# Optimization experiments

Measured on AMD Instinct MI355X. Metric: run time of the kernel, lower is better.

## Reference

```python
import jax, jax.numpy as jnp
import numpy as np

# ---- config (JambaConfig defaults) ----
D_MODEL = 2048
D_STATE = 128
D_CONV = 4
EXPAND = 2
HEADDIM = 64
D_INNER = EXPAND * D_MODEL           # 4096
NHEADS = D_INNER // HEADDIM          # 64
CONV_DIM = D_INNER + 2 * D_STATE     # 4352
IN_PROJ = 2 * D_INNER + 2 * D_STATE + NHEADS  # 8512
INTER = 5632                         # ((2048*8/3)+255)//256*256
EPS = 1e-6
CHUNK = 128                          # SSD chunk length


def rmsnorm(x, w, eps=EPS):
    var = jnp.mean(jnp.square(x), axis=-1, keepdims=True)
    return x * jax.lax.rsqrt(var + eps) * w


def dw_causal_conv(x, w, b):
    # x: [B,L,C], w: [C,K] depthwise, b: [C]; causal (left pad K-1)
    xt = jnp.transpose(x, (0, 2, 1))                       # [B,C,L]
    xt = jnp.pad(xt, ((0, 0), (0, 0), (D_CONV - 1, 0)))
    y = jax.lax.conv_general_dilated(
        xt, w[:, None, :], window_strides=(1,), padding='VALID',
        feature_group_count=w.shape[0], dimension_numbers=('NCH', 'OIH', 'NCH'))
    y = y + b[None, :, None]
    return jnp.transpose(y, (0, 2, 1))                     # [B,L,C]


def segsum(x):
    # x: [..., T] -> [..., T, T] with out[l,s] = sum_{s<i<=l} x[i], -inf above diag
    T = x.shape[-1]
    xx = jnp.broadcast_to(x[..., None], (*x.shape, T))     # xx[...,i,j] = x[...,i]
    xx = jnp.where(jnp.tril(jnp.ones((T, T), bool), -1), xx, 0.0)
    s = jnp.cumsum(xx, axis=-2)
    return jnp.where(jnp.tril(jnp.ones((T, T), bool), 0), s, -jnp.inf)


def ssd(x, dt, A, Bm, Cm):
    # Mamba2 SSD (chunked selective scan). x:[b,l,h,p] dt:[b,l,h] A:[h] Bm/Cm:[b,l,n]
    b, l, h, p = x.shape
    n = Bm.shape[-1]
    c = l // CHUNK
    xr = x.reshape(b, c, CHUNK, h, p)
    dtr = dt.reshape(b, c, CHUNK, h)
    Br = Bm.reshape(b, c, CHUNK, n)
    Cr = Cm.reshape(b, c, CHUNK, n)
    dA = jnp.transpose(dtr * A, (0, 3, 1, 2))              # [b,h,c,q], all <= 0
    A_cum = jnp.cumsum(dA, axis=-1)                        # [b,h,c,q]
    L = jnp.exp(segsum(dA))                                # [b,h,c,q,q] lower-tri decays
    xdt = xr * dtr[..., None]                              # [b,c,q,h,p]
    # intra-chunk (diagonal blocks)
    Y_diag = jnp.einsum('bcln,bcsn,bhcls,bcshp->bclhp', Cr, Br, L, xdt)
    # chunk-final states
    decay_states = jnp.exp(A_cum[..., -1:] - A_cum)        # [b,h,c,q]
    states = jnp.einsum('bcln,bhcl,bclhp->bchpn', Br, decay_states, xdt)
    # inter-chunk recurrence (parallel via decay matrix over chunks)
    A_last = A_cum[..., -1]                                # [b,h,c]
    decay_chunk = jnp.exp(segsum(jnp.pad(A_last, ((0, 0), (0, 0), (1, 0)))))  # [b,h,c+1,c+1]
    states_cat = jnp.concatenate([jnp.zeros_like(states[:, :1]), states], axis=1)  # [b,c+1,h,p,n]
    new_states = jnp.einsum('bhzc,bchpn->bzhpn', decay_chunk, states_cat)
    prev = new_states[:, :-1]                              # state entering each chunk
    state_decay = jnp.exp(A_cum)                           # [b,h,c,q]
    Y_off = jnp.einsum('bcln,bchpn,bhcl->bclhp', Cr, prev, state_decay)
    return (Y_diag + Y_off).reshape(b, l, h, p)


def setup_inputs() -> dict:
    key = jax.random.key(0)
    ks = jax.random.split(key, 10)
    B, L = 2, 2048
    s = 0.02
    return {
        'hidden_states': jax.random.normal(ks[0], (B, L, D_MODEL), jnp.float32),
        'norm1_w': jnp.ones((D_MODEL,), jnp.float32),
        'in_proj_w': jax.random.normal(ks[1], (D_MODEL, IN_PROJ), jnp.float32) * s,
        'conv_w': jax.random.normal(ks[2], (CONV_DIM, D_CONV), jnp.float32) * 0.1,
        'conv_b': jnp.zeros((CONV_DIM,), jnp.float32),
        'dt_bias': jax.random.uniform(ks[3], (NHEADS,), jnp.float32, -4.0, -1.0),
        'A_log': jnp.log(jnp.arange(1, NHEADS + 1, dtype=jnp.float32)),
        'D_param': jnp.ones((NHEADS,), jnp.float32),
        'mixer_norm_w': jnp.ones((D_INNER,), jnp.float32),
        'out_proj_w': jax.random.normal(ks[4], (D_INNER, D_MODEL), jnp.float32) * s,
        'norm2_w': jnp.ones((D_MODEL,), jnp.float32),
        'gate_w': jax.random.normal(ks[5], (D_MODEL, INTER), jnp.float32) * s,
        'up_w': jax.random.normal(ks[6], (D_MODEL, INTER), jnp.float32) * s,
        'down_w': jax.random.normal(ks[7], (INTER, D_MODEL), jnp.float32) * s,
    }


def reference(hidden_states, norm1_w, in_proj_w, conv_w, conv_b, dt_bias, A_log,
              D_param, mixer_norm_w, out_proj_w, norm2_w, gate_w, up_w, down_w):
    B, L, _ = hidden_states.shape
    # --- norm1 + Mamba2 mixer + residual ---
    res = hidden_states
    h = rmsnorm(hidden_states, norm1_w)
    zxbcdt = h @ in_proj_w                                  # [B,L,8512]
    z = zxbcdt[..., :D_INNER]
    xBC = zxbcdt[..., D_INNER:D_INNER + CONV_DIM]
    dt = jax.nn.softplus(zxbcdt[..., -NHEADS:] + dt_bias)   # [B,L,H]
    xBC = jax.nn.silu(dw_causal_conv(xBC, conv_w, conv_b))
    xs = xBC[..., :D_INNER].reshape(B, L, NHEADS, HEADDIM)
    Bm = xBC[..., D_INNER:D_INNER + D_STATE]
    Cm = xBC[..., D_INNER + D_STATE:]
    A = -jnp.exp(A_log)
    y = ssd(xs, dt, A, Bm, Cm)
    y = y + D_param[None, None, :, None] * xs               # skip D term
    y = y.reshape(B, L, D_INNER)
    y = rmsnorm(y * jax.nn.silu(z), mixer_norm_w)           # gated RMSNorm
    h1 = res + y @ out_proj_w
    # --- norm2 + SwiGLU MLP + residual ---
    h2 = rmsnorm(h1, norm2_w)
    mlp = (jax.nn.silu(h2 @ gate_w) * (h2 @ up_w)) @ down_w
    return h1 + mlp
```

## Files before the change

kernel.cpp:

```cpp
#include <hip/hip_runtime.h>

#define LTOT 2048
#define BATCH 2
#define NTOK 4096
#define DMODEL 2048
#define DSTATE 128
#define NH 64
#define HD 64
#define DINNER 4096
#define CONVD 4352
#define XDTC 4416
#define INP 8512
#define INTER_ 5632
#define CHUNK_ 128
#define NCH 16
#define EPSF 1e-6f

typedef __bf16 bf16x8 __attribute__((ext_vector_type(8)));
typedef float f32x4 __attribute__((ext_vector_type(4)));
typedef unsigned short u16x4 __attribute__((ext_vector_type(4)));
typedef unsigned short u16x8 __attribute__((ext_vector_type(8)));

__device__ __forceinline__ unsigned short f2b(float f){
  unsigned int u = __builtin_bit_cast(unsigned int, f);
  u += 0x7fffu + ((u >> 16) & 1u);
  return (unsigned short)(u >> 16);
}
__device__ __forceinline__ float b2f(unsigned short h){
  return __builtin_bit_cast(float, ((unsigned int)h) << 16);
}
__device__ __forceinline__ f32x4 mfma16(bf16x8 a, bf16x8 b, f32x4 c){
  return __builtin_amdgcn_mfma_f32_16x16x32_bf16(a, b, c, 0, 0, 0);
}
typedef const __attribute__((address_space(1))) void* gas_t;
typedef __attribute__((address_space(3))) void* las_t;
__device__ __forceinline__ void gload16(const void* g, void* l){
  __builtin_amdgcn_global_load_lds((gas_t)g, (las_t)l, 16, 0, 0);
}

__global__ __launch_bounds__(256) void wconv_kernel(const float* __restrict__ W,
                                                    unsigned short* __restrict__ WT,
                                                    int K, int N)
{
  __shared__ unsigned short t[64][72];
  int n0 = blockIdx.x * 64, k0 = blockIdx.y * 64;
  int tid = threadIdx.x;
  int kl = tid >> 4, nl4 = (tid & 15) * 4;
  #pragma unroll
  for (int it = 0; it < 4; it++){
    int kk = kl + it * 16;
    float4 v = make_float4(0.f, 0.f, 0.f, 0.f);
    if (n0 < N) v = *(const float4*)&W[(size_t)(k0 + kk) * N + n0 + nl4];
    t[nl4 + 0][kk] = f2b(v.x);
    t[nl4 + 1][kk] = f2b(v.y);
    t[nl4 + 2][kk] = f2b(v.z);
    t[nl4 + 3][kk] = f2b(v.w);
  }
  __syncthreads();
  int nr = tid >> 3, k8 = (tid & 7) * 8;
  #pragma unroll
  for (int it = 0; it < 2; it++){
    int nn = nr + it * 32;
    *(u16x8*)&WT[(size_t)(n0 + nn) * K + k0 + k8] = *(const u16x8*)&t[nn][k8];
  }
}

__global__ __launch_bounds__(256) void rms_kernel(const float* __restrict__ x,
                                                  const float* __restrict__ w,
                                                  unsigned short* __restrict__ out, int width)
{
  int row = blockIdx.x, tid = threadIdx.x;
  const float* xr = x + (size_t)row * width;
  unsigned short* orow = out + (size_t)row * width;
  int nv = width >> 2;
  float ss = 0.f;
  for (int i = tid; i < nv; i += 256){
    float4 v = ((const float4*)xr)[i];
    ss += v.x*v.x + v.y*v.y + v.z*v.z + v.w*v.w;
  }
  #pragma unroll
  for (int off = 32; off > 0; off >>= 1) ss += __shfl_down(ss, off, 64);
  __shared__ float red[4];
  if ((tid & 63) == 0) red[tid >> 6] = ss;
  __syncthreads();
  float tot = red[0] + red[1] + red[2] + red[3];
  float scale = rsqrtf(tot / (float)width + EPSF);
  for (int i = tid; i < nv; i += 256){
    float4 v = ((const float4*)xr)[i];
    float4 wv = ((const float4*)w)[i];
    u16x4 o = { f2b(v.x * scale * wv.x), f2b(v.y * scale * wv.y),
                f2b(v.z * scale * wv.z), f2b(v.w * scale * wv.w) };
    ((u16x4*)orow)[i] = o;
  }
}

__global__ __launch_bounds__(256) void rms_gated_kernel(const float* __restrict__ y,
                                                        const unsigned short* __restrict__ z,
                                                        const float* __restrict__ w,
                                                        unsigned short* __restrict__ out)
{
  int row = blockIdx.x, tid = threadIdx.x;
  const float* yr = y + (size_t)row * DINNER;
  const unsigned short* zr = z + (size_t)row * DINNER;
  unsigned short* orow = out + (size_t)row * DINNER;
  float g[16];
  float ss = 0.f;
  #pragma unroll
  for (int ii = 0; ii < 4; ii++){
    int i = tid + ii * 256;
    float4 yv = ((const float4*)yr)[i];
    u16x4 zv = ((const u16x4*)zr)[i];
    #pragma unroll
    for (int e = 0; e < 4; e++){
      float zf = b2f(zv[e]);
      float yf = (&yv.x)[e];
      float gg = yf * (zf / (1.f + expf(-zf)));
      g[ii * 4 + e] = gg;
      ss += gg * gg;
    }
  }
  #pragma unroll
  for (int off = 32; off > 0; off >>= 1) ss += __shfl_down(ss, off, 64);
  __shared__ float red[4];
  if ((tid & 63) == 0) red[tid >> 6] = ss;
  __syncthreads();
  float tot = red[0] + red[1] + red[2] + red[3];
  float scale = rsqrtf(tot / (float)DINNER + EPSF);
  #pragma unroll
  for (int ii = 0; ii < 4; ii++){
    int i = tid + ii * 256;
    float4 wv = ((const float4*)w)[i];
    u16x4 o;
    #pragma unroll
    for (int e = 0; e < 4; e++) o[e] = f2b(g[ii * 4 + e] * scale * (&wv.x)[e]);
    ((u16x4*)orow)[i] = o;
  }
}

__global__ __launch_bounds__(256) void act_kernel(unsigned short* __restrict__ g,
                                                  const unsigned short* __restrict__ u, int n8)
{
  int stride = gridDim.x * 256;
  for (int i = blockIdx.x * 256 + threadIdx.x; i < n8; i += stride){
    u16x8 gv = ((const u16x8*)g)[i];
    u16x8 uv = ((const u16x8*)u)[i];
    u16x8 o;
    #pragma unroll
    for (int e = 0; e < 8; e++){
      float gf = b2f(gv[e]);
      o[e] = f2b(gf / (1.f + expf(-gf)) * b2f(uv[e]));
    }
    ((u16x8*)g)[i] = o;
  }
}

__global__ __launch_bounds__(512, 2) void gemm3_kernel(const unsigned short* __restrict__ A,
                                                       const unsigned short* __restrict__ BT,
                                                       const float* __restrict__ addsrc,
                                                       float* __restrict__ Cf,
                                                       unsigned short* __restrict__ Cb,
                                                       unsigned short* __restrict__ Cb2, int splitN,
                                                       const unsigned short* __restrict__ gate,
                                                       float* __restrict__ dtraw,
                                                       int M, int N, int K)
{
  extern __shared__ unsigned short lds[];
  int tid = threadIdx.x, lane = tid & 63, w = tid >> 6;
  int wm = w >> 2, wn = w & 3;
  int bid = blockIdx.x + blockIdx.y * gridDim.x;
  int nwg = gridDim.x * gridDim.y;
  int q8 = nwg >> 3, r8 = nwg & 7;
  int xcd = bid & 7, boff = bid >> 3;
  int wgid = (xcd < r8 ? xcd * (q8 + 1) : r8 * (q8 + 1) + (xcd - r8) * q8) + boff;
  int bn = (wgid % gridDim.x) * 256;
  int bm = (wgid / gridDim.x) * 128;

  int soct8 = ((lane & 3) ^ ((lane >> 2) & 3)) << 3;
  int prow_l = (lane >> 2);
  int ko = (((lane >> 4) ^ (lane & 3)) << 3);
  int rsel = (lane & 15) * 32 + ko;

  f32x4 acc[4][4] = {};
  int NT = K >> 5;

  #define STAGE(kt, bsel)                                                              \
    {                                                                                  \
      unsigned short* bb_ = &lds[(bsel) * 12288];                                      \
      size_t k0_ = (size_t)(kt) << 5;                                                  \
      gload16(&A [(size_t)(bm +       w * 16 + prow_l) * K + k0_ + soct8], &bb_[w * 512]);            \
      gload16(&BT[(size_t)(bn +       w * 16 + prow_l) * K + k0_ + soct8], &bb_[4096 + w * 512]);     \
      gload16(&BT[(size_t)(bn + 128 + w * 16 + prow_l) * K + k0_ + soct8], &bb_[8192 + w * 512]);     \
    }

  STAGE(0, 0)
  STAGE(1, 1)
  asm volatile("s_waitcnt vmcnt(3)" ::: "memory");
  __builtin_amdgcn_s_barrier();
  asm volatile("" ::: "memory");

  for (int t = 0; t < NT; ++t){
    const unsigned short* bufc = &lds[(t % 3) * 12288];
    bf16x8 afr[4], bfr[4];
    #pragma unroll
    for (int i = 0; i < 4; ++i)
      afr[i] = *(const bf16x8*)&bufc[(wm * 64 + i * 16) * 32 + rsel];
    #pragma unroll
    for (int c = 0; c < 4; ++c)
      bfr[c] = *(const bf16x8*)&bufc[4096 + (wn * 64 + c * 16) * 32 + rsel];
    if (t + 2 < NT) STAGE(t + 2, (t + 2) % 3)
    __builtin_amdgcn_s_setprio(1);
    #pragma unroll
    for (int i = 0; i < 4; ++i)
      #pragma unroll
      for (int c = 0; c < 4; ++c)
        acc[i][c] = mfma16(afr[i], bfr[c], acc[i][c]);
    __builtin_amdgcn_s_setprio(0);
    if (t + 2 < NT)      asm volatile("s_waitcnt vmcnt(3)" ::: "memory");
    else if (t + 1 < NT) asm volatile("s_waitcnt vmcnt(0)" ::: "memory");
    asm volatile("" ::: "memory");
    __builtin_amdgcn_s_barrier();
    asm volatile("" ::: "memory");
  }
  #undef STAGE

  int r0 = bm + wm * 64 + ((lane >> 4) << 2);
  int c0 = bn + wn * 64 + (lane & 15);
  #pragma unroll
  for (int i = 0; i < 4; ++i){
    #pragma unroll
    for (int j = 0; j < 4; ++j){
      int cc = c0 + j * 16;
      if (cc < N){
        #pragma unroll
        for (int e = 0; e < 4; ++e){
          int rr = r0 + i * 16 + e;
          float v = acc[i][j][e];
          if (Cf){
            size_t idx = (size_t)rr * N + cc;
            if (addsrc) v += addsrc[idx];
            Cf[idx] = v;
          } else if (cc < splitN){
            size_t idx = (size_t)rr * splitN + cc;
            float vv = v;
            if (gate){ float gg = b2f(gate[idx]); vv = gg / (1.f + expf(-gg)) * v; }
            Cb[idx] = f2b(vv);
          } else {
            Cb2[(size_t)rr * (N - splitN) + (cc - splitN)] = f2b(v);
            if (dtraw && cc >= N - NH) dtraw[(size_t)rr * NH + (cc - (N - NH))] = v;
          }
        }
      }
    }
  }
}

__global__ __launch_bounds__(256, 3) void gemm4_kernel(const unsigned short* __restrict__ A,
                                                       const unsigned short* __restrict__ BT,
                                                       const float* __restrict__ addsrc,
                                                       float* __restrict__ Cf,
                                                       int M, int N, int K)
{
  extern __shared__ unsigned short lds[];
  int tid = threadIdx.x, lane = tid & 63, w = tid >> 6;
  int wm = w >> 1, wn = w & 1;
  int bid = blockIdx.x + blockIdx.y * gridDim.x;
  int nwg = gridDim.x * gridDim.y;
  int q8 = nwg >> 3, r8 = nwg & 7;
  int xcd = bid & 7, boff = bid >> 3;
  int wgid = (xcd < r8 ? xcd * (q8 + 1) : r8 * (q8 + 1) + (xcd - r8) * q8) + boff;
  int bn = (wgid % gridDim.x) * 128;
  int bm = (wgid / gridDim.x) * 128;

  int soct8 = ((lane & 3) ^ ((lane >> 2) & 3)) << 3;
  int prow_l = (lane >> 2);
  int ko = (((lane >> 4) ^ (lane & 3)) << 3);
  int rsel = (lane & 15) * 32 + ko;

  f32x4 acc[4][4] = {};
  int NT = K >> 5;

  #define STAGE4(kt, bsel)                                                             \
    {                                                                                  \
      unsigned short* bb_ = &lds[(bsel) * 8192];                                       \
      size_t k0_ = (size_t)(kt) << 5;                                                  \
      gload16(&A [(size_t)(bm +      w * 16 + prow_l) * K + k0_ + soct8], &bb_[w * 512]);          \
      gload16(&A [(size_t)(bm + 64 + w * 16 + prow_l) * K + k0_ + soct8], &bb_[2048 + w * 512]);   \
      gload16(&BT[(size_t)(bn +      w * 16 + prow_l) * K + k0_ + soct8], &bb_[4096 + w * 512]);   \
      gload16(&BT[(size_t)(bn + 64 + w * 16 + prow_l) * K + k0_ + soct8], &bb_[6144 + w * 512]);   \
    }

  STAGE4(0, 0)
  STAGE4(1, 1)
  asm volatile("s_waitcnt vmcnt(4)" ::: "memory");
  __builtin_amdgcn_s_barrier();
  asm volatile("" ::: "memory");

  for (int t = 0; t < NT; ++t){
    const unsigned short* bufc = &lds[(t % 3) * 8192];
    bf16x8 afr[4], bfr[4];
    #pragma unroll
    for (int i = 0; i < 4; ++i)
      afr[i] = *(const bf16x8*)&bufc[(wm * 64 + i * 16) * 32 + rsel];
    #pragma unroll
    for (int c = 0; c < 4; ++c)
      bfr[c] = *(const bf16x8*)&bufc[4096 + (wn * 64 + c * 16) * 32 + rsel];
    if (t + 2 < NT) STAGE4(t + 2, (t + 2) % 3)
    __builtin_amdgcn_s_setprio(1);
    #pragma unroll
    for (int i = 0; i < 4; ++i)
      #pragma unroll
      for (int c = 0; c < 4; ++c)
        acc[i][c] = mfma16(afr[i], bfr[c], acc[i][c]);
    __builtin_amdgcn_s_setprio(0);
    if (t + 2 < NT)      asm volatile("s_waitcnt vmcnt(4)" ::: "memory");
    else if (t + 1 < NT) asm volatile("s_waitcnt vmcnt(0)" ::: "memory");
    asm volatile("" ::: "memory");
    __builtin_amdgcn_s_barrier();
    asm volatile("" ::: "memory");
  }
  #undef STAGE4

  int r0 = bm + wm * 64 + ((lane >> 4) << 2);
  int c0 = bn + wn * 64 + (lane & 15);
  #pragma unroll
  for (int i = 0; i < 4; ++i){
    #pragma unroll
    for (int j = 0; j < 4; ++j){
      int cc = c0 + j * 16;
      #pragma unroll
      for (int e = 0; e < 4; ++e){
        int rr = r0 + i * 16 + e;
        size_t idx = (size_t)rr * N + cc;
        float v = acc[i][j][e];
        if (addsrc) v += addsrc[idx];
        Cf[idx] = v;
      }
    }
  }
}

__global__ __launch_bounds__(256) void dt_kernel(const float* __restrict__ dtraw,
                                                 const float* __restrict__ dt_bias,
                                                 float* __restrict__ dtb)
{
  int idx = blockIdx.x * 256 + threadIdx.x;
  float raw = dtraw[idx] + dt_bias[idx & 63];
  dtb[idx] = (raw > 20.f) ? raw : log1pf(expf(raw));
}

__global__ __launch_bounds__(64) void acum_kernel(const float* __restrict__ dtb,
                                                  const float* __restrict__ A_log,
                                                  float* __restrict__ acum)
{
  int bid = blockIdx.x;
  int c = bid & 15;
  int hh = (bid >> 4) & 63;
  int b = bid >> 10;
  int lane = threadIdx.x;
  float Av = -expf(A_log[hh]);
  int rowbase = b * LTOT + c * CHUNK_;
  float v0 = dtb[(size_t)(rowbase + 2 * lane) * NH + hh] * Av;
  float v1 = dtb[(size_t)(rowbase + 2 * lane + 1) * NH + hh] * Av;
  float s = v0 + v1;
  #pragma unroll
  for (int d = 1; d < 64; d <<= 1){
    float t = __shfl_up(s, d, 64);
    if (lane >= d) s += t;
  }
  float excl = s - (v0 + v1);
  float* dst = acum + ((size_t)(b * NH + hh)) * LTOT + c * CHUNK_;
  dst[2 * lane]     = excl + v0;
  dst[2 * lane + 1] = excl + v0 + v1;
}

__global__ __launch_bounds__(256) void conv_kernel(const unsigned short* __restrict__ xdt,
                                                   const float* __restrict__ cw,
                                                   const float* __restrict__ cb,
                                                   unsigned short* __restrict__ xbc)
{
  int ch = blockIdx.x * 256 + threadIdx.x;
  int l0 = blockIdx.y * 4, b = blockIdx.z;
  float x[7];
  #pragma unroll
  for (int j = 0; j < 7; j++){
    int ls = l0 - 3 + j;
    x[j] = (ls >= 0) ? b2f(xdt[((size_t)(b * LTOT + ls)) * XDTC + ch]) : 0.f;
  }
  float w0 = cw[ch * 4 + 0], w1 = cw[ch * 4 + 1], w2 = cw[ch * 4 + 2], w3 = cw[ch * 4 + 3];
  float bias = cb[ch];
  #pragma unroll
  for (int i = 0; i < 4; i++){
    float acc = bias + x[i] * w0 + x[i + 1] * w1 + x[i + 2] * w2 + x[i + 3] * w3;
    acc = acc / (1.f + expf(-acc));
    xbc[((size_t)(b * LTOT + l0 + i)) * CONVD + ch] = f2b(acc);
  }
}

__global__ __launch_bounds__(256) void ssd_sy_kernel(const unsigned short* __restrict__ xbc,
                                                     const float* __restrict__ dtb,
                                                     const float* __restrict__ acum,
                                                     float* __restrict__ y)
{
  int hh = blockIdx.x;
  int c = blockIdx.y >> 1;
  int half = blockIdx.y & 1;
  int b = blockIdx.z;
  __shared__ unsigned short Cs[64][136];
  __shared__ unsigned short Bs[128][136];
  __shared__ float ac[128];
  int tid = threadIdx.x, lane = tid & 63, w = tid >> 6;
  int l0 = half * 64;
  size_t rowbase = (size_t)b * LTOT + c * CHUNK_;
  if (tid < 128) ac[tid] = acum[((size_t)(b * NH + hh)) * LTOT + c * CHUNK_ + tid];
  #pragma unroll
  for (int p = 0; p < 8; p++){
    int lr = p * 8 + (tid >> 5);
    int n4 = (tid & 31) * 4;
    *(u16x4*)&Cs[lr][n4] =
      *(const u16x4*)&xbc[(rowbase + l0 + lr) * CONVD + DINNER + DSTATE + n4];
  }
  #pragma unroll
  for (int p = 0; p < 16; p++){
    int s = p * 8 + (tid >> 5);
    int n4 = (tid & 31) * 4;
    *(u16x4*)&Bs[s][n4] = *(const u16x4*)&xbc[(rowbase + s) * CONVD + DINNER + n4];
  }
  __syncthreads();
  f32x4 accS[8] = {};
  #pragma unroll
  for (int kk = 0; kk < 4; kk++){
    bf16x8 a = *(const bf16x8*)&Cs[w * 16 + (lane & 15)][kk * 32 + (lane >> 4) * 8];
    #pragma unroll
    for (int fc = 0; fc < 8; fc++){
      bf16x8 bb = *(const bf16x8*)&Bs[fc * 16 + (lane & 15)][kk * 32 + (lane >> 4) * 8];
      accS[fc] = mfma16(a, bb, accS[fc]);
    }
  }
  __syncthreads();
  {
    int lr = w * 16 + ((lane >> 4) << 2);
    #pragma unroll
    for (int fc = 0; fc < 8; fc++){
      int s = fc * 16 + (lane & 15);
      #pragma unroll
      for (int j = 0; j < 4; j++){
        int l = l0 + lr + j;
        float v = (s <= l) ? accS[fc][j] * expf(ac[l] - ac[s]) : 0.f;
        Cs[lr + j][s] = f2b(v);
      }
    }
  }
  #pragma unroll
  for (int p = 0; p < 8; p++){
    int lr = p * 16 + (tid >> 4);
    int p4 = (tid & 15) * 4;
    float dtl = dtb[(rowbase + lr) * NH + hh];
    u16x4 v = *(const u16x4*)&xbc[(rowbase + lr) * CONVD + hh * HD + p4];
    Bs[p4 + 0][lr] = f2b(b2f(v[0]) * dtl);
    Bs[p4 + 1][lr] = f2b(b2f(v[1]) * dtl);
    Bs[p4 + 2][lr] = f2b(b2f(v[2]) * dtl);
    Bs[p4 + 3][lr] = f2b(b2f(v[3]) * dtl);
  }
  __syncthreads();
  f32x4 accY[4] = {};
  #pragma unroll
  for (int kk = 0; kk < 4; kk++){
    bf16x8 a = *(const bf16x8*)&Cs[w * 16 + (lane & 15)][kk * 32 + (lane >> 4) * 8];
    #pragma unroll
    for (int fc = 0; fc < 4; fc++){
      bf16x8 bb = *(const bf16x8*)&Bs[fc * 16 + (lane & 15)][kk * 32 + (lane >> 4) * 8];
      accY[fc] = mfma16(a, bb, accY[fc]);
    }
  }
  {
    int lr = w * 16 + ((lane >> 4) << 2);
    #pragma unroll
    for (int fc = 0; fc < 4; fc++){
      int p = fc * 16 + (lane & 15);
      #pragma unroll
      for (int j = 0; j < 4; j++){
        y[(rowbase + l0 + lr + j) * DINNER + hh * HD + p] = accY[fc][j];
      }
    }
  }
}

__global__ __launch_bounds__(256) void ssd_states_kernel(const unsigned short* __restrict__ xbc,
                                                         const float* __restrict__ dtb,
                                                         const float* __restrict__ acum,
                                                         unsigned short* __restrict__ states)
{
  int hh = blockIdx.x, c = blockIdx.y, b = blockIdx.z;
  __shared__ unsigned short BsT[128][136];
  __shared__ unsigned short XT[64][136];
  __shared__ float ac[128];
  int tid = threadIdx.x, lane = tid & 63, w = tid >> 6;
  size_t rowbase = (size_t)b * LTOT + c * CHUNK_;
  if (tid < 128) ac[tid] = acum[((size_t)(b * NH + hh)) * LTOT + c * CHUNK_ + tid];
  #pragma unroll
  for (int p = 0; p < 16; p++){
    int l = p * 8 + (tid >> 5);
    int n4 = (tid & 31) * 4;
    u16x4 v = *(const u16x4*)&xbc[(rowbase + l) * CONVD + DINNER + n4];
    BsT[n4 + 0][l] = v[0];
    BsT[n4 + 1][l] = v[1];
    BsT[n4 + 2][l] = v[2];
    BsT[n4 + 3][l] = v[3];
  }
  #pragma unroll
  for (int p = 0; p < 8; p++){
    int l = p * 16 + (tid >> 4);
    int p4 = (tid & 15) * 4;
    float dtl = dtb[(rowbase + l) * NH + hh];
    u16x4 v = *(const u16x4*)&xbc[(rowbase + l) * CONVD + hh * HD + p4];
    XT[p4 + 0][l] = f2b(b2f(v[0]) * dtl);
    XT[p4 + 1][l] = f2b(b2f(v[1]) * dtl);
    XT[p4 + 2][l] = f2b(b2f(v[2]) * dtl);
    XT[p4 + 3][l] = f2b(b2f(v[3]) * dtl);
  }
  __syncthreads();
  float aclast = ac[127];
  f32x4 accP[8] = {};
  #pragma unroll
  for (int kk = 0; kk < 4; kk++){
    int kbase = kk * 32 + (lane >> 4) * 8;
    union { u16x4 q[2]; unsigned short u[8]; bf16x8 v; } rw, ot;
    rw.q[0] = *(const u16x4*)&XT[w * 16 + (lane & 15)][kbase];
    rw.q[1] = *(const u16x4*)&XT[w * 16 + (lane & 15)][kbase + 4];
    #pragma unroll
    for (int e = 0; e < 8; e++){
      ot.u[e] = f2b(b2f(rw.u[e]) * expf(aclast - ac[kbase + e]));
    }
    #pragma unroll
    for (int fc = 0; fc < 8; fc++){
      bf16x8 bb = *(const bf16x8*)&BsT[fc * 16 + (lane & 15)][kbase];
      accP[fc] = mfma16(ot.v, bb, accP[fc]);
    }
  }
  size_t sbase = ((size_t)((b * NCH + c) * NH + hh)) * HD * DSTATE;
  int p0 = w * 16 + ((lane >> 4) << 2);
  #pragma unroll
  for (int fc = 0; fc < 8; fc++){
    int n = fc * 16 + (lane & 15);
    #pragma unroll
    for (int j = 0; j < 4; j++){
      states[sbase + (size_t)(p0 + j) * DSTATE + n] = f2b(accP[fc][j]);
    }
  }
}

__global__ __launch_bounds__(256) void scan_kernel(unsigned short* __restrict__ states,
                                                   const float* __restrict__ acum)
{
  int bh = blockIdx.x;
  int b = bh >> 6, hh = bh & 63;
  int jg = blockIdx.y * 4;
  int t = threadIdx.x;
  float run[4] = {0.f, 0.f, 0.f, 0.f};
  for (int c = 0; c < NCH; c++){
    float alast = acum[(size_t)bh * LTOT + c * CHUNK_ + 127];
    float dec = expf(alast);
    size_t base = ((size_t)((b * NCH + c) * NH + hh)) * (HD * DSTATE);
    #pragma unroll
    for (int j = 0; j < 4; j++){
      size_t idx = base + (size_t)(jg + j) * 256 + t;
      float sc = b2f(states[idx]);
      states[idx] = f2b(run[j]);
      run[j] = run[j] * dec + sc;
    }
  }
}

__global__ __launch_bounds__(256) void ssd3_kernel(const unsigned short* __restrict__ xbc,
                                                   const unsigned short* __restrict__ states,
                                                   const float* __restrict__ acum,
                                                   const float* __restrict__ Dp,
                                                   float* __restrict__ y)
{
  int hh = blockIdx.x, c = blockIdx.y, b = blockIdx.z;
  __shared__ unsigned short Cs[128][136];
  __shared__ unsigned short Ps[64][136];
  __shared__ float ac[128];
  int tid = threadIdx.x, lane = tid & 63, w = tid >> 6;
  size_t rowbase = (size_t)b * LTOT + c * CHUNK_;
  if (tid < 128) ac[tid] = acum[((size_t)(b * NH + hh)) * LTOT + c * CHUNK_ + tid];
  #pragma unroll
  for (int p = 0; p < 16; p++){
    int l = p * 8 + (tid >> 5);
    int n4 = (tid & 31) * 4;
    *(u16x4*)&Cs[l][n4] =
      *(const u16x4*)&xbc[(rowbase + l) * CONVD + DINNER + DSTATE + n4];
  }
  size_t sbase = ((size_t)((b * NCH + c) * NH + hh)) * (HD * DSTATE);
  #pragma unroll
  for (int p = 0; p < 8; p++){
    int pp = p * 8 + (tid >> 5);
    int n4 = (tid & 31) * 4;
    *(u16x4*)&Ps[pp][n4] = *(const u16x4*)&states[sbase + (size_t)pp * DSTATE + n4];
  }
  __syncthreads();
  f32x4 acc[2][4] = {};
  #pragma unroll
  for (int kk = 0; kk < 4; kk++){
    bf16x8 a0 = *(const bf16x8*)&Cs[w * 32 + (lane & 15)][kk * 32 + (lane >> 4) * 8];
    bf16x8 a1 = *(const bf16x8*)&Cs[w * 32 + 16 + (lane & 15)][kk * 32 + (lane >> 4) * 8];
    #pragma unroll
    for (int fc = 0; fc < 4; fc++){
      bf16x8 bb = *(const bf16x8*)&Ps[fc * 16 + (lane & 15)][kk * 32 + (lane >> 4) * 8];
      acc[0][fc] = mfma16(a0, bb, acc[0][fc]);
      acc[1][fc] = mfma16(a1, bb, acc[1][fc]);
    }
  }
  float dpar = Dp[hh];
  #pragma unroll
  for (int fr = 0; fr < 2; fr++){
    int lr = w * 32 + fr * 16 + ((lane >> 4) << 2);
    #pragma unroll
    for (int fc = 0; fc < 4; fc++){
      int p = fc * 16 + (lane & 15);
      #pragma unroll
      for (int j = 0; j < 4; j++){
        int l = lr + j;
        size_t yi = (rowbase + l) * DINNER + hh * HD + p;
        float xsv = b2f(xbc[(rowbase + l) * CONVD + hh * HD + p]);
        y[yi] += acc[fr][fc][j] * expf(ac[l]) + dpar * xsv;
      }
    }
  }
}

extern "C" void kernel_launch(void* const* d_in, const int* in_sizes, int n_in,
                              void* d_out, int out_size, void* d_ws, size_t ws_size,
                              hipStream_t stream)
{
  (void)in_sizes; (void)n_in; (void)out_size; (void)ws_size;
  const float* hidden    = (const float*)d_in[0];
  const float* norm1_w   = (const float*)d_in[1];
  const float* in_proj_w = (const float*)d_in[2];
  const float* conv_w    = (const float*)d_in[3];
  const float* conv_b    = (const float*)d_in[4];
  const float* dt_bias   = (const float*)d_in[5];
  const float* A_log     = (const float*)d_in[6];
  const float* D_param   = (const float*)d_in[7];
  const float* mixer_w   = (const float*)d_in[8];
  const float* out_proj_w= (const float*)d_in[9];
  const float* norm2_w   = (const float*)d_in[10];
  const float* gate_w    = (const float*)d_in[11];
  const float* up_w      = (const float*)d_in[12];
  const float* down_w    = (const float*)d_in[13];

  char* ws = (char*)d_ws;
  unsigned short* zbuf    = (unsigned short*)(ws);
  unsigned short* WT_cat  = (unsigned short*)(ws);
  unsigned short* WT_down = (unsigned short*)(ws);
  unsigned short* xdt     = (unsigned short*)(ws + 33554432ull);
  unsigned short* states  = (unsigned short*)(ws + 33554432ull);
  unsigned short* ygn     = (unsigned short*)(ws + 33554432ull);
  unsigned short* ubuf    = (unsigned short*)(ws + 46137344ull);
  unsigned short* xbc     = (unsigned short*)(ws + 69730304ull);
  unsigned short* WT_out  = (unsigned short*)(ws + 69730304ull);
  float* dtraw            = (float*)(ws + 105381888ull);
  float* dtb              = (float*)(ws + 106430464ull);
  float* acum             = (float*)(ws + 107479040ull);
  float* ybuf             = (float*)(ws + 108527616ull);
  unsigned short* hbuf    = (unsigned short*)(ws + 108527616ull);
  unsigned short* gbuf    = (unsigned short*)(ws + 108527616ull);
  unsigned short* WT_in   = (unsigned short*)(ws + 125304832ull);
  unsigned short* h2      = (unsigned short*)(ws + 154664960ull);
  float* h1               = (float*)d_out;
  float* outp             = (float*)d_out;

  const int dynLDS3 = 73728;
  const int dynLDS4 = 49152;
  hipFuncSetAttribute((const void*)gemm3_kernel,
                      hipFuncAttributeMaxDynamicSharedMemorySize, dynLDS3);
  hipFuncSetAttribute((const void*)gemm4_kernel,
                      hipFuncAttributeMaxDynamicSharedMemorySize, dynLDS4);

  wconv_kernel<<<dim3(136, 32), 256, 0, stream>>>(in_proj_w, WT_in, DMODEL, INP);
  rms_kernel<<<NTOK, 256, 0, stream>>>(hidden, norm1_w, hbuf, DMODEL);
  gemm3_kernel<<<dim3(34, 32), 512, dynLDS3, stream>>>(hbuf, WT_in, nullptr, nullptr,
                                                       zbuf, xdt, DINNER, nullptr, dtraw,
                                                       NTOK, INP, DMODEL);
  dt_kernel<<<NTOK * NH / 256, 256, 0, stream>>>(dtraw, dt_bias, dtb);
  acum_kernel<<<BATCH * NH * NCH, 64, 0, stream>>>(dtb, A_log, acum);
  conv_kernel<<<dim3(CONVD / 256, LTOT / 4, BATCH), 256, 0, stream>>>(xdt, conv_w, conv_b, xbc);
  ssd_sy_kernel<<<dim3(NH, NCH * 2, BATCH), 256, 0, stream>>>(xbc, dtb, acum, ybuf);
  ssd_states_kernel<<<dim3(NH, NCH, BATCH), 256, 0, stream>>>(xbc, dtb, acum, states);
  scan_kernel<<<dim3(BATCH * NH, 8), 256, 0, stream>>>(states, acum);
  ssd3_kernel<<<dim3(NH, NCH, BATCH), 256, 0, stream>>>(xbc, states, acum, D_param, ybuf);
  rms_gated_kernel<<<NTOK, 256, 0, stream>>>(ybuf, zbuf, mixer_w, ygn);
  wconv_kernel<<<dim3(32, 64), 256, 0, stream>>>(out_proj_w, WT_out, DINNER, DMODEL);
  gemm4_kernel<<<dim3(16, 32), 256, dynLDS4, stream>>>(ygn, WT_out, hidden, h1,
                                                       NTOK, DMODEL, DINNER);
  rms_kernel<<<NTOK, 256, 0, stream>>>(h1, norm2_w, h2, DMODEL);
  wconv_kernel<<<dim3(88, 32), 256, 0, stream>>>(gate_w, WT_cat, DMODEL, INTER_);
  wconv_kernel<<<dim3(88, 32), 256, 0, stream>>>(up_w, WT_cat + 11534336ull, DMODEL, INTER_);
  gemm3_kernel<<<dim3(44, 32), 512, dynLDS3, stream>>>(h2, WT_cat, nullptr, nullptr,
                                                       gbuf, ubuf, INTER_, nullptr, nullptr,
                                                       NTOK, 2 * INTER_, DMODEL);
  act_kernel<<<2048, 256, 0, stream>>>(gbuf, ubuf, NTOK * INTER_ / 8);
  wconv_kernel<<<dim3(32, 88), 256, 0, stream>>>(down_w, WT_down, INTER_, DMODEL);
  gemm4_kernel<<<dim3(16, 32), 256, dynLDS4, stream>>>(gbuf, WT_down, h1, outp,
                                                       NTOK, DMODEL, INTER_);
}
```

Before: 1.012 ms.

## Enlarge in-proj and MLP GEMM tiles to 256x256 and revise LDS swizzle

The 512-thread GEMM moves from a 128x256 to a 256x256 output tile, with each wave holding 8x4 accumulators. Each staged K-slice is reused across twice as many rows, which halves global and LDS traffic per FLOP. In exchange, occupancy drops to one workgroup per CU with 96KB of LDS, and the M grid is halved, giving fewer workgroups (544 and 704) across the CUs and a possible wave-quantization tail. The LDS XOR swizzle is also changed in both GEMM kernels to add a row-dependent term, aimed at reducing bank conflicts on the fragment reads.

```diff
diff --git a/kernel.cpp b/kernel.cpp
--- a/kernel.cpp
+++ b/kernel.cpp
@@ -38,6 +38,7 @@
   __builtin_amdgcn_global_load_lds((gas_t)g, (las_t)l, 16, 0, 0);
 }
 
+
 __global__ __launch_bounds__(256) void wconv_kernel(const float* __restrict__ W,
                                                     unsigned short* __restrict__ WT,
                                                     int K, int N)
@@ -154,7 +155,7 @@
   }
 }
 
-__global__ __launch_bounds__(512, 2) void gemm3_kernel(const unsigned short* __restrict__ A,
+__global__ __launch_bounds__(512, 1) void gemm8_kernel(const unsigned short* __restrict__ A,
                                                        const unsigned short* __restrict__ BT,
                                                        const float* __restrict__ addsrc,
                                                        float* __restrict__ Cf,
@@ -173,60 +174,63 @@
   int xcd = bid & 7, boff = bid >> 3;
   int wgid = (xcd < r8 ? xcd * (q8 + 1) : r8 * (q8 + 1) + (xcd - r8) * q8) + boff;
   int bn = (wgid % gridDim.x) * 256;
-  int bm = (wgid / gridDim.x) * 128;
-
-  int soct8 = ((lane & 3) ^ ((lane >> 2) & 3)) << 3;
-  int prow_l = (lane >> 2);
-  int ko = (((lane >> 4) ^ (lane & 3)) << 3);
+  int bm = (wgid / gridDim.x) * 256;
+
+  int gsrc = (((lane & 3) ^ ((lane >> 2) & 3) ^ ((4 * w + (lane >> 4)) & 3)) << 3);
+  int prow_l = lane >> 2;
+  int ko = (((lane >> 4) ^ (lane & 3) ^ ((lane >> 2) & 3)) << 3);
   int rsel = (lane & 15) * 32 + ko;
 
-  f32x4 acc[4][4] = {};
+  f32x4 acc[8][4] = {};
   int NT = K >> 5;
 
-  #define STAGE(kt, bsel)                                                              \
-    {                                                                                  \
-      unsigned short* bb_ = &lds[(bsel) * 12288];                                      \
-      size_t k0_ = (size_t)(kt) << 5;                                                  \
-      gload16(&A [(size_t)(bm +       w * 16 + prow_l) * K + k0_ + soct8], &bb_[w * 512]);            \
-      gload16(&BT[(size_t)(bn +       w * 16 + prow_l) * K + k0_ + soct8], &bb_[4096 + w * 512]);     \
-      gload16(&BT[(size_t)(bn + 128 + w * 16 + prow_l) * K + k0_ + soct8], &bb_[8192 + w * 512]);     \
-    }
-
-  STAGE(0, 0)
-  STAGE(1, 1)
-  asm volatile("s_waitcnt vmcnt(3)" ::: "memory");
+  #define STAGE8(kt, bsel)                                                                   \
+    {                                                                                        \
+      unsigned short* bA_ = &lds[(bsel) * 16384];                                            \
+      unsigned short* bB_ = bA_ + 8192;                                                      \
+      size_t k0_ = (size_t)(kt) << 5;                                                        \
+      gload16(&A [(size_t)(bm +       w * 16 + prow_l) * K + k0_ + gsrc], &bA_[w * 512]);    \
+      gload16(&A [(size_t)(bm + 128 + w * 16 + prow_l) * K + k0_ + gsrc], &bA_[4096 + w * 512]); \
+      gload16(&BT[(size_t)(bn +       w * 16 + prow_l) * K + k0_ + gsrc], &bB_[w * 512]);    \
+      gload16(&BT[(size_t)(bn + 128 + w * 16 + prow_l) * K + k0_ + gsrc], &bB_[4096 + w * 512]); \
+    }
+
+  STAGE8(0, 0)
+  STAGE8(1, 1)
+  asm volatile("s_waitcnt vmcnt(4)" ::: "memory");
   __builtin_amdgcn_s_barrier();
   asm volatile("" ::: "memory");
 
   for (int t = 0; t < NT; ++t){
-    const unsigned short* bufc = &lds[(t % 3) * 12288];
-    bf16x8 afr[4], bfr[4];
-    #pragma unroll
-    for (int i = 0; i < 4; ++i)
-      afr[i] = *(const bf16x8*)&bufc[(wm * 64 + i * 16) * 32 + rsel];
+    const unsigned short* bA = &lds[(t % 3) * 16384];
+    const unsigned short* bB = bA + 8192;
+    bf16x8 afr[8], bfr[4];
+    #pragma unroll
+    for (int i = 0; i < 8; ++i)
+      afr[i] = *(const bf16x8*)&bA[(wm * 128 + i * 16) * 32 + rsel];
     #pragma unroll
     for (int c = 0; c < 4; ++c)
-      bfr[c] = *(const bf16x8*)&bufc[4096 + (wn * 64 + c * 16) * 32 + rsel];
-    if (t + 2 < NT) STAGE(t + 2, (t + 2) % 3)
+      bfr[c] = *(const bf16x8*)&bB[(wn * 64 + c * 16) * 32 + rsel];
+    if (t + 2 < NT) STAGE8(t + 2, (t + 2) % 3)
     __builtin_amdgcn_s_setprio(1);
     #pragma unroll
-    for (int i = 0; i < 4; ++i)
+    for (int i = 0; i < 8; ++i)
       #pragma unroll
       for (int c = 0; c < 4; ++c)
         acc[i][c] = mfma16(afr[i], bfr[c], acc[i][c]);
     __builtin_amdgcn_s_setprio(0);
-    if (t + 2 < NT)      asm volatile("s_waitcnt vmcnt(3)" ::: "memory");
+    if (t + 2 < NT)      asm volatile("s_waitcnt vmcnt(4)" ::: "memory");
     else if (t + 1 < NT) asm volatile("s_waitcnt vmcnt(0)" ::: "memory");
     asm volatile("" ::: "memory");
     __builtin_amdgcn_s_barrier();
     asm volatile("" ::: "memory");
   }
-  #undef STAGE
-
-  int r0 = bm + wm * 64 + ((lane >> 4) << 2);
+  #undef STAGE8
+
+  int r0 = bm + wm * 128 + ((lane >> 4) << 2);
   int c0 = bn + wn * 64 + (lane & 15);
   #pragma unroll
-  for (int i = 0; i < 4; ++i){
+  for (int i = 0; i < 8; ++i){
     #pragma unroll
     for (int j = 0; j < 4; ++j){
       int cc = c0 + j * 16;
@@ -271,9 +275,9 @@
   int bn = (wgid % gridDim.x) * 128;
   int bm = (wgid / gridDim.x) * 128;
 
-  int soct8 = ((lane & 3) ^ ((lane >> 2) & 3)) << 3;
-  int prow_l = (lane >> 2);
-  int ko = (((lane >> 4) ^ (lane & 3)) << 3);
+  int gsrc = (((lane & 3) ^ ((lane >> 2) & 3) ^ ((4 * w + (lane >> 4)) & 3)) << 3);
+  int prow_l = lane >> 2;
+  int ko = (((lane >> 4) ^ (lane & 3) ^ ((lane >> 2) & 3)) << 3);
   int rsel = (lane & 15) * 32 + ko;
 
   f32x4 acc[4][4] = {};
@@ -283,10 +287,10 @@
     {                                                                                  \
       unsigned short* bb_ = &lds[(bsel) * 8192];                                       \
       size_t k0_ = (size_t)(kt) << 5;                                                  \
-      gload16(&A [(size_t)(bm +      w * 16 + prow_l) * K + k0_ + soct8], &bb_[w * 512]);          \
-      gload16(&A [(size_t)(bm + 64 + w * 16 + prow_l) * K + k0_ + soct8], &bb_[2048 + w * 512]);   \
-      gload16(&BT[(size_t)(bn +      w * 16 + prow_l) * K + k0_ + soct8], &bb_[4096 + w * 512]);   \
-      gload16(&BT[(size_t)(bn + 64 + w * 16 + prow_l) * K + k0_ + soct8], &bb_[6144 + w * 512]);   \
+      gload16(&A [(size_t)(bm +      w * 16 + prow_l) * K + k0_ + gsrc], &bb_[w * 512]);          \
+      gload16(&A [(size_t)(bm + 64 + w * 16 + prow_l) * K + k0_ + gsrc], &bb_[2048 + w * 512]);   \
+      gload16(&BT[(size_t)(bn +      w * 16 + prow_l) * K + k0_ + gsrc], &bb_[4096 + w * 512]);   \
+      gload16(&BT[(size_t)(bn + 64 + w * 16 + prow_l) * K + k0_ + gsrc], &bb_[6144 + w * 512]);   \
     }
 
   STAGE4(0, 0)
@@ -670,16 +674,16 @@
   float* h1               = (float*)d_out;
   float* outp             = (float*)d_out;
 
-  const int dynLDS3 = 73728;
+  const int dynLDS8 = 98304;
   const int dynLDS4 = 49152;
-  hipFuncSetAttribute((const void*)gemm3_kernel,
-                      hipFuncAttributeMaxDynamicSharedMemorySize, dynLDS3);
+  hipFuncSetAttribute((const void*)gemm8_kernel,
+                      hipFuncAttributeMaxDynamicSharedMemorySize, dynLDS8);
   hipFuncSetAttribute((const void*)gemm4_kernel,
                       hipFuncAttributeMaxDynamicSharedMemorySize, dynLDS4);
 
   wconv_kernel<<<dim3(136, 32), 256, 0, stream>>>(in_proj_w, WT_in, DMODEL, INP);
   rms_kernel<<<NTOK, 256, 0, stream>>>(hidden, norm1_w, hbuf, DMODEL);
-  gemm3_kernel<<<dim3(34, 32), 512, dynLDS3, stream>>>(hbuf, WT_in, nullptr, nullptr,
+  gemm8_kernel<<<dim3(34, 16), 512, dynLDS8, stream>>>(hbuf, WT_in, nullptr, nullptr,
                                                        zbuf, xdt, DINNER, nullptr, dtraw,
                                                        NTOK, INP, DMODEL);
   dt_kernel<<<NTOK * NH / 256, 256, 0, stream>>>(dtraw, dt_bias, dtb);
@@ -696,7 +700,7 @@
   rms_kernel<<<NTOK, 256, 0, stream>>>(h1, norm2_w, h2, DMODEL);
   wconv_kernel<<<dim3(88, 32), 256, 0, stream>>>(gate_w, WT_cat, DMODEL, INTER_);
   wconv_kernel<<<dim3(88, 32), 256, 0, stream>>>(up_w, WT_cat + 11534336ull, DMODEL, INTER_);
-  gemm3_kernel<<<dim3(44, 32), 512, dynLDS3, stream>>>(h2, WT_cat, nullptr, nullptr,
+  gemm8_kernel<<<dim3(44, 16), 512, dynLDS8, stream>>>(h2, WT_cat, nullptr, nullptr,
                                                        gbuf, ubuf, INTER_, nullptr, nullptr,
                                                        NTOK, 2 * INTER_, DMODEL);
   act_kernel<<<2048, 256, 0, stream>>>(gbuf, ubuf, NTOK * INTER_ / 8);
```

Measured after the change: 1.100 ms. +8.7%, slower.
